# Optimization experiments

Measured on AMD Instinct MI355X. Metric: run time of the kernel, lower is better.

## Reference

```python
import jax, jax.numpy as jnp
import numpy as np

N_QUBITS = 4
N_LAYERS = 3
H_IMG = 512

# ---------- 4-qubit statevector simulator, batched over P patches ----------

def _apply_1q(psi, U, w):
    # shared 2x2 gate U on wire w; psi: (P,2,2,2,2)
    psi = jnp.moveaxis(psi, 1 + w, -1)
    psi = jnp.einsum('ij,...j->...i', U, psi)
    return jnp.moveaxis(psi, -1, 1 + w)

def _apply_1q_batched(psi, U, w):
    # per-patch gate U: (P,2,2)
    psi = jnp.moveaxis(psi, 1 + w, -1)
    psi = jnp.einsum('pij,p...j->p...i', U, psi)
    return jnp.moveaxis(psi, -1, 1 + w)

def _apply_cnot(psi, c, t):
    psi = jnp.moveaxis(psi, (1 + c, 1 + t), (-2, -1))
    top = psi[..., 0:1, :]
    bot = psi[..., 1:2, ::-1]  # X on target when control=1
    psi = jnp.concatenate([top, bot], axis=-2)
    return jnp.moveaxis(psi, (-2, -1), (1 + c, 1 + t))

def _rx(theta):
    # AngleEmbedding default rotation='X'; theta: (P,) -> (P,2,2)
    h = theta * 0.5
    c = jnp.cos(h).astype(jnp.complex64)
    s = (-1j * jnp.sin(h)).astype(jnp.complex64)
    return jnp.stack([jnp.stack([c, s], -1), jnp.stack([s, c], -1)], -2)

def _rot(phi, theta, omega):
    # PennyLane Rot = RZ(omega) RY(theta) RZ(phi)
    c = jnp.cos(theta * 0.5)
    s = jnp.sin(theta * 0.5)
    em = jnp.exp(-0.5j * (phi + omega))
    ep = jnp.exp(0.5j * (phi + omega))
    fm = jnp.exp(0.5j * (phi - omega))
    fp = jnp.exp(-0.5j * (phi - omega))
    row0 = jnp.stack([em * c, -fm * s])
    row1 = jnp.stack([fp * s, ep * c])
    return jnp.stack([row0, row1]).astype(jnp.complex64)

def _qsim(inputs, weights):
    # inputs: (P,4) angles; weights: (3,4,3) Rot params -> (P,4) PauliZ expvals
    P = inputs.shape[0]
    psi = jnp.zeros((P, 2, 2, 2, 2), jnp.complex64).at[:, 0, 0, 0, 0].set(1.0)
    for w in range(N_QUBITS):
        psi = _apply_1q_batched(psi, _rx(inputs[:, w]), w)
    for l in range(N_LAYERS):
        for w in range(N_QUBITS):
            psi = _apply_1q(psi, _rot(weights[l, w, 0], weights[l, w, 1], weights[l, w, 2]), w)
        r = (l % (N_QUBITS - 1)) + 1  # StronglyEntanglingLayers default ranges
        for w in range(N_QUBITS):
            psi = _apply_cnot(psi, w, (w + r) % N_QUBITS)
    probs = psi.real ** 2 + psi.imag ** 2  # (P,2,2,2,2)
    ez = []
    for w in range(N_QUBITS):
        axes = tuple(a for a in range(1, 5) if a != 1 + w)
        p = probs.sum(axes)  # (P,2)
        ez.append(p[:, 0] - p[:, 1])
    return jnp.stack(ez, -1)  # (P,4)

def _qconv(x, q_weights):
    img = x[0, 0]  # (H,W)
    a = img[:-1, :-1]; b = img[:-1, 1:]; c = img[1:, :-1]; d = img[1:, 1:]
    Hm, Wm = a.shape
    patches = jnp.stack([a, b, c, d], -1).reshape(-1, 4)  # row-major 2x2 flatten
    ez = _qsim(patches, q_weights)  # (P,4)
    return ez.reshape(Hm, Wm, 4).transpose(2, 0, 1)[None]  # (1,4,Hm,Wm)

# ---------- classical layers ----------

def _conv(x, w, b):
    y = jax.lax.conv_general_dilated(x, w, (1, 1), 'VALID',
                                     dimension_numbers=('NCHW', 'OIHW', 'NCHW'))
    return y + b[None, :, None, None]

def _maxpool2(x):
    return jax.lax.reduce_window(x, -jnp.inf, jax.lax.max,
                                 (1, 1, 2, 2), (1, 1, 2, 2), 'VALID')

def _adaptive_max(x, out):
    H, W = x.shape[-2], x.shape[-1]
    rows = []
    for i in range(out):
        si, ei = (i * H) // out, -(-((i + 1) * H) // out)
        cols = []
        for j in range(out):
            sj, ej = (j * W) // out, -(-((j + 1) * W) // out)
            cols.append(x[..., si:ei, sj:ej].max((-2, -1)))
        rows.append(jnp.stack(cols, -1))
    return jnp.stack(rows, -2)


def setup_inputs() -> dict:
    key = jax.random.key(0)
    ks = jax.random.split(key, 10)
    x = jax.random.normal(ks[0], (1, 1, H_IMG, H_IMG), jnp.float32)
    q_weights = jax.random.uniform(ks[1], (N_LAYERS, N_QUBITS, 3), jnp.float32,
                                   0.0, 2.0 * np.pi)
    conv2_w = jax.random.normal(ks[2], (20, 4, 5, 5), jnp.float32) * 0.05
    conv2_b = jax.random.normal(ks[3], (20,), jnp.float32) * 0.05
    conv3_w = jax.random.normal(ks[4], (40, 20, 3, 3), jnp.float32) * 0.05
    conv3_b = jax.random.normal(ks[5], (40,), jnp.float32) * 0.05
    fc1_w = jax.random.normal(ks[6], (64, 640), jnp.float32) * 0.05
    fc1_b = jax.random.normal(ks[7], (64,), jnp.float32) * 0.05
    fc2_w = jax.random.normal(ks[8], (10, 64), jnp.float32) * 0.05
    fc2_b = jax.random.normal(ks[9], (10,), jnp.float32) * 0.05
    return {'x': x, 'q_weights': q_weights,
            'conv2_w': conv2_w, 'conv2_b': conv2_b,
            'conv3_w': conv3_w, 'conv3_b': conv3_b,
            'fc1_w': fc1_w, 'fc1_b': fc1_b,
            'fc2_w': fc2_w, 'fc2_b': fc2_b}


def reference(x, q_weights, conv2_w, conv2_b, conv3_w, conv3_b,
              fc1_w, fc1_b, fc2_w, fc2_b):
    h = _maxpool2(jax.nn.sigmoid(_qconv(x, q_weights)))        # (1,4,255,255)
    h = _maxpool2(jax.nn.relu(_conv(h, conv2_w, conv2_b)))      # (1,20,125,125)
    h = _adaptive_max(jax.nn.relu(_conv(h, conv3_w, conv3_b)), 4)  # (1,40,4,4)
    h = h.reshape(-1, 640)
    h = jax.nn.relu(h @ fc1_w.T + fc1_b)
    return h @ fc2_w.T + fc2_b  # (1,10)
```

## Files before the change

### kernel.cpp

```cpp
#include <hip/hip_runtime.h>
#include <math.h>

#define IMG 512
#define QO  255

__global__ void build_M(const float* __restrict__ qw, float2* __restrict__ Mout) {
    __shared__ float2 A[16][16];
    int tid = threadIdx.x;
    for (int e = tid; e < 256; e += 128) {
        int col = e >> 4, row = e & 15;
        A[col][row] = make_float2(col == row ? 1.f : 0.f, 0.f);
    }
    __syncthreads();

    int col = tid >> 3;
    int p   = tid & 7;

    for (int l = 0; l < 3; ++l) {
        for (int w = 0; w < 4; ++w) {
            float phi = qw[(l*4 + w)*3 + 0];
            float th  = qw[(l*4 + w)*3 + 1];
            float om  = qw[(l*4 + w)*3 + 2];
            float ch = cosf(0.5f*th), sh = sinf(0.5f*th);
            float al = 0.5f*(phi + om), be = 0.5f*(phi - om);
            float ca = cosf(al), sa = sinf(al);
            float cb = cosf(be), sb = sinf(be);
            float2 U00 = make_float2( ca*ch, -sa*ch);
            float2 U01 = make_float2(-cb*sh, -sb*sh);
            float2 U10 = make_float2( cb*sh, -sb*sh);
            float2 U11 = make_float2( ca*ch,  sa*ch);

            int bp = 3 - w, m = 1 << bp;
            int low = p & (m - 1);
            int k0  = ((p ^ low) << 1) | low;
            int k1  = k0 | m;
            float2 a0 = A[col][k0], a1 = A[col][k1];
            float2 n0 = make_float2(U00.x*a0.x - U00.y*a0.y + U01.x*a1.x - U01.y*a1.y,
                                    U00.x*a0.y + U00.y*a0.x + U01.x*a1.y + U01.y*a1.x);
            float2 n1 = make_float2(U10.x*a0.x - U10.y*a0.y + U11.x*a1.x - U11.y*a1.y,
                                    U10.x*a0.y + U10.y*a0.x + U11.x*a1.y + U11.y*a1.x);
            A[col][k0] = n0;
            A[col][k1] = n1;
            __syncthreads();
        }
        int r = l % 3 + 1;
        for (int w = 0; w < 4; ++w) {
            int cq = w, tq = (w + r) & 3;
            int bpc = 3 - cq, bpt = 3 - tq;
            if (p < 4) {
                int fr0 = -1, fr1 = -1;
                for (int b = 0; b < 4; ++b) {
                    if (b != bpc && b != bpt) { if (fr0 < 0) fr0 = b; else fr1 = b; }
                }
                int k  = (1 << bpc) | ((p & 1) << fr0) | (((p >> 1) & 1) << fr1);
                int k2 = k | (1 << bpt);
                float2 t = A[col][k]; A[col][k] = A[col][k2]; A[col][k2] = t;
            }
            __syncthreads();
        }
    }

    for (int e = tid; e < 256; e += 128) {
        int row = e >> 4, k = e & 15;
        float2 v = A[k][row];
        int pc = __popc(k) & 3;
        float2 o;
        if      (pc == 0) o = v;
        else if (pc == 1) o = make_float2( v.y, -v.x);
        else if (pc == 2) o = make_float2(-v.x, -v.y);
        else              o = make_float2(-v.y,  v.x);
        Mout[e] = o;
    }
}

__global__ __launch_bounds__(256) void qconv_pool(const float* __restrict__ img,
                                                  const float2* __restrict__ Mg,
                                                  float* __restrict__ out) {
    __shared__ float2 Ms[256];
    int tid = threadIdx.x;
    Ms[tid] = Mg[tid];
    __syncthreads();

    int gid = blockIdx.x * 256 + tid;
    if (gid >= QO * QO) return;
    int i = gid / QO, j = gid - i * QO;
    int r0 = 2 * i, c0col = 2 * j;

    float cs[3][3], sn[3][3];
    #pragma unroll
    for (int rr = 0; rr < 3; ++rr) {
        #pragma unroll
        for (int cc = 0; cc < 3; ++cc) {
            float v = img[(r0 + rr) * IMG + c0col + cc];
            __sincosf(0.5f * v, &sn[rr][cc], &cs[rr][cc]);
        }
    }

    float mx0 = -1e30f, mx1 = -1e30f, mx2 = -1e30f, mx3 = -1e30f;

    #pragma unroll
    for (int pr = 0; pr < 2; ++pr) {
        #pragma unroll
        for (int pc = 0; pc < 2; ++pc) {
            float c0 = cs[pr][pc],     s0 = sn[pr][pc];
            float c1 = cs[pr][pc+1],   s1 = sn[pr][pc+1];
            float c2 = cs[pr+1][pc],   s2 = sn[pr+1][pc];
            float c3 = cs[pr+1][pc+1], s3 = sn[pr+1][pc+1];
            float t01[4] = {c0*c1, c0*s1, s0*c1, s0*s1};
            float t23[4] = {c2*c3, c2*s3, s2*c3, s2*s3};
            float a[16];
            #pragma unroll
            for (int k = 0; k < 16; ++k) a[k] = t01[k >> 2] * t23[k & 3];

            float e0 = 0.f, e1 = 0.f, e2 = 0.f, e3 = 0.f;
            for (int rw = 0; rw < 16; ++rw) {
                float re = 0.f, im = 0.f;
                #pragma unroll
                for (int k = 0; k < 16; ++k) {
                    float2 m = Ms[rw * 16 + k];
                    re = fmaf(m.x, a[k], re);
                    im = fmaf(m.y, a[k], im);
                }
                float pp = re * re + im * im;
                e0 += (rw & 8) ? -pp : pp;
                e1 += (rw & 4) ? -pp : pp;
                e2 += (rw & 2) ? -pp : pp;
                e3 += (rw & 1) ? -pp : pp;
            }
            mx0 = fmaxf(mx0, e0);
            mx1 = fmaxf(mx1, e1);
            mx2 = fmaxf(mx2, e2);
            mx3 = fmaxf(mx3, e3);
        }
    }

    out[0 * QO * QO + gid] = 1.f / (1.f + __expf(-mx0));
    out[1 * QO * QO + gid] = 1.f / (1.f + __expf(-mx1));
    out[2 * QO * QO + gid] = 1.f / (1.f + __expf(-mx2));
    out[3 * QO * QO + gid] = 1.f / (1.f + __expf(-mx3));
}

__global__ __launch_bounds__(256) void conv2_pool(const float* __restrict__ in,
                                                  const float* __restrict__ w,
                                                  const float* __restrict__ b,
                                                  float* __restrict__ out) {
    __shared__ float W[2000];
    __shared__ float B[20];
    for (int e = threadIdx.x; e < 2000; e += 256) W[e] = w[e];
    if (threadIdx.x < 20) B[threadIdx.x] = b[threadIdx.x];
    __syncthreads();

    int gid = blockIdx.x * 256 + threadIdx.x;
    if (gid >= 20 * 125 * 125) return;
    int oc = gid / (125 * 125);
    int rem = gid - oc * 125 * 125;
    int i = rem / 125, j = rem - i * 125;

    float a00 = 0.f, a01 = 0.f, a10 = 0.f, a11 = 0.f;
    for (int ic = 0; ic < 4; ++ic) {
        const float* ip = in + ic * QO * QO + (2 * i) * QO + 2 * j;
        float win[6][6];
        #pragma unroll
        for (int y = 0; y < 6; ++y)
            #pragma unroll
            for (int x = 0; x < 6; ++x)
                win[y][x] = ip[y * QO + x];
        const float* wp = W + (oc * 4 + ic) * 25;
        #pragma unroll
        for (int ky = 0; ky < 5; ++ky) {
            #pragma unroll
            for (int kx = 0; kx < 5; ++kx) {
                float wv = wp[ky * 5 + kx];
                a00 = fmaf(win[ky][kx],     wv, a00);
                a01 = fmaf(win[ky][kx+1],   wv, a01);
                a10 = fmaf(win[ky+1][kx],   wv, a10);
                a11 = fmaf(win[ky+1][kx+1], wv, a11);
            }
        }
    }
    float m = fmaxf(fmaxf(a00, a01), fmaxf(a10, a11));
    out[gid] = fmaxf(m + B[oc], 0.f);
}

__global__ __launch_bounds__(256) void conv3_k(const float* __restrict__ in,
                                               const float* __restrict__ w,
                                               const float* __restrict__ b,
                                               float* __restrict__ out) {
    __shared__ float4 W4[1800];
    for (int e = threadIdx.x; e < 1800; e += 256) {
        int og = e / 180, rr = e - og * 180;
        int base = (og * 4) * 180 + rr;
        W4[e] = make_float4(w[base], w[base + 180], w[base + 360], w[base + 540]);
    }
    __syncthreads();

    int gid = blockIdx.x * 256 + threadIdx.x;
    if (gid >= 10 * 123 * 123) return;
    int og = gid / (123 * 123);
    int rem = gid - og * (123 * 123);
    int y = rem / 123, x = rem - y * 123;
    int oc0 = og * 4;

    float acc0 = 0.f, acc1 = 0.f, acc2 = 0.f, acc3 = 0.f;
    for (int ic = 0; ic < 20; ++ic) {
        const float* ip = in + ic * 125 * 125 + y * 125 + x;
        float v[3][3];
        #pragma unroll
        for (int ky = 0; ky < 3; ++ky)
            #pragma unroll
            for (int kx = 0; kx < 3; ++kx)
                v[ky][kx] = ip[ky * 125 + kx];
        #pragma unroll
        for (int ky = 0; ky < 3; ++ky) {
            #pragma unroll
            for (int kx = 0; kx < 3; ++kx) {
                float4 wv = W4[og * 180 + ic * 9 + ky * 3 + kx];
                float iv = v[ky][kx];
                acc0 = fmaf(iv, wv.x, acc0);
                acc1 = fmaf(iv, wv.y, acc1);
                acc2 = fmaf(iv, wv.z, acc2);
                acc3 = fmaf(iv, wv.w, acc3);
            }
        }
    }
    int sp = y * 123 + x;
    out[(oc0 + 0) * 123 * 123 + sp] = fmaxf(acc0 + b[oc0 + 0], 0.f);
    out[(oc0 + 1) * 123 * 123 + sp] = fmaxf(acc1 + b[oc0 + 1], 0.f);
    out[(oc0 + 2) * 123 * 123 + sp] = fmaxf(acc2 + b[oc0 + 2], 0.f);
    out[(oc0 + 3) * 123 * 123 + sp] = fmaxf(acc3 + b[oc0 + 3], 0.f);
}

__global__ void amax_k(const float* __restrict__ in, float* __restrict__ out) {
    int ob = blockIdx.x;
    int oc = ob >> 4, bi = (ob >> 2) & 3, bj = ob & 3;
    int y0 = (bi * 123) >> 2, y1 = ((bi + 1) * 123 + 3) >> 2;
    int x0 = (bj * 123) >> 2, x1 = ((bj + 1) * 123 + 3) >> 2;
    int ny = y1 - y0, nx = x1 - x0, tot = ny * nx;
    float m = -1e30f;
    for (int e = threadIdx.x; e < tot; e += 64) {
        int yy = e / nx, xx = e - yy * nx;
        m = fmaxf(m, in[oc * 123 * 123 + (y0 + yy) * 123 + x0 + xx]);
    }
    #pragma unroll
    for (int o = 32; o > 0; o >>= 1) m = fmaxf(m, __shfl_down(m, o, 64));
    if (threadIdx.x == 0) out[ob] = m;
}

__global__ void fc_k(const float* __restrict__ h, const float* __restrict__ w1,
                     const float* __restrict__ b1, const float* __restrict__ w2,
                     const float* __restrict__ b2, float* __restrict__ out) {
    __shared__ float hh[640];
    __shared__ float h1[64];
    int t = threadIdx.x;
    for (int e = t; e < 640; e += 64) hh[e] = h[e];
    __syncthreads();
    float acc = b1[t];
    for (int n = 0; n < 640; ++n) acc = fmaf(hh[n], w1[t * 640 + n], acc);
    h1[t] = fmaxf(acc, 0.f);
    __syncthreads();
    if (t < 10) {
        float o = b2[t];
        for (int n = 0; n < 64; ++n) o = fmaf(h1[n], w2[t * 64 + n], o);
        out[t] = o;
    }
}

extern "C" void kernel_launch(void* const* d_in, const int* in_sizes, int n_in,
                              void* d_out, int out_size, void* d_ws, size_t ws_size,
                              hipStream_t stream) {
    const float* x   = (const float*)d_in[0];
    const float* qw  = (const float*)d_in[1];
    const float* c2w = (const float*)d_in[2];
    const float* c2b = (const float*)d_in[3];
    const float* c3w = (const float*)d_in[4];
    const float* c3b = (const float*)d_in[5];
    const float* f1w = (const float*)d_in[6];
    const float* f1b = (const float*)d_in[7];
    const float* f2w = (const float*)d_in[8];
    const float* f2b = (const float*)d_in[9];
    float* out = (float*)d_out;

    float*  wsf   = (float*)d_ws;
    float2* M     = (float2*)d_ws;
    float*  qout  = wsf + 512;
    float*  c2out = qout + 4 * 255 * 255;
    float*  c3out = c2out + 20 * 125 * 125;
    float*  am    = c3out + 40 * 123 * 123;

    build_M<<<1, 128, 0, stream>>>(qw, M);
    qconv_pool<<<(QO * QO + 255) / 256, 256, 0, stream>>>(x, M, qout);
    conv2_pool<<<(20 * 125 * 125 + 255) / 256, 256, 0, stream>>>(qout, c2w, c2b, c2out);
    conv3_k<<<(10 * 123 * 123 + 255) / 256, 256, 0, stream>>>(c2out, c3w, c3b, c3out);
    amax_k<<<640, 64, 0, stream>>>(c3out, am);
    fc_k<<<1, 64, 0, stream>>>(am, f1w, f1b, f2w, f2b, out);
}
```

Baseline: 132.6 us.

## Pad intermediate layouts, read weights uniformly, and register-simulate the circuit matrix

Intermediate feature maps now use padded row strides (256 and 128), so conv2 can issue float2 window loads and rows are aligned. The conv kernels index output channels by blockIdx.y and read weights directly from global memory, where each block's addresses are uniform, replacing the shared-memory staging and its syncs. qconv reads the 16x16 unitary from global instead of LDS. build_M simulates each column in registers with compile-time gates, and fc1 splits each dot product over four lanes with float4 loads. The risk is that global weight reads go through the scalar/L1 path instead of LDS, which may be slower in the hot qconv loop.

```diff
diff --git a/kernel.cpp b/kernel.cpp
--- a/kernel.cpp
+++ b/kernel.cpp
@@ -3,98 +3,92 @@
 
 #define IMG 512
 #define QO  255
+#define QP  256
+#define C2H 125
+#define C2S 128
+#define C3H 123
+#define C3S 128
+
+template<int M_>
+__device__ inline void rot_regs(float2* a, float2 U00, float2 U01, float2 U10, float2 U11) {
+    #pragma unroll
+    for (int s = 0; s < 16; ++s) {
+        if (!(s & M_)) {
+            float2 a0 = a[s], a1 = a[s | M_];
+            a[s]      = make_float2(U00.x*a0.x - U00.y*a0.y + U01.x*a1.x - U01.y*a1.y,
+                                    U00.x*a0.y + U00.y*a0.x + U01.x*a1.y + U01.y*a1.x);
+            a[s | M_] = make_float2(U10.x*a0.x - U10.y*a0.y + U11.x*a1.x - U11.y*a1.y,
+                                    U10.x*a0.y + U10.y*a0.x + U11.x*a1.y + U11.y*a1.x);
+        }
+    }
+}
+template<int MC, int MT>
+__device__ inline void cnot_regs(float2* a) {
+    #pragma unroll
+    for (int s = 0; s < 16; ++s) {
+        if ((s & MC) && !(s & MT)) {
+            float2 t = a[s]; a[s] = a[s | MT]; a[s | MT] = t;
+        }
+    }
+}
+__device__ inline void rot_gate_params(float phi, float th, float om,
+                                       float2& U00, float2& U01, float2& U10, float2& U11) {
+    float ch, sh, ca, sa, cb, sb;
+    __sincosf(0.5f * th, &sh, &ch);
+    __sincosf(0.5f * (phi + om), &sa, &ca);
+    __sincosf(0.5f * (phi - om), &sb, &cb);
+    U00 = make_float2( ca*ch, -sa*ch);
+    U01 = make_float2(-cb*sh, -sb*sh);
+    U10 = make_float2( cb*sh, -sb*sh);
+    U11 = make_float2( ca*ch,  sa*ch);
+}
 
 __global__ void build_M(const float* __restrict__ qw, float2* __restrict__ Mout) {
-    __shared__ float2 A[16][16];
-    int tid = threadIdx.x;
-    for (int e = tid; e < 256; e += 128) {
-        int col = e >> 4, row = e & 15;
-        A[col][row] = make_float2(col == row ? 1.f : 0.f, 0.f);
-    }
-    __syncthreads();
-
-    int col = tid >> 3;
-    int p   = tid & 7;
-
-    for (int l = 0; l < 3; ++l) {
-        for (int w = 0; w < 4; ++w) {
-            float phi = qw[(l*4 + w)*3 + 0];
-            float th  = qw[(l*4 + w)*3 + 1];
-            float om  = qw[(l*4 + w)*3 + 2];
-            float ch = cosf(0.5f*th), sh = sinf(0.5f*th);
-            float al = 0.5f*(phi + om), be = 0.5f*(phi - om);
-            float ca = cosf(al), sa = sinf(al);
-            float cb = cosf(be), sb = sinf(be);
-            float2 U00 = make_float2( ca*ch, -sa*ch);
-            float2 U01 = make_float2(-cb*sh, -sb*sh);
-            float2 U10 = make_float2( cb*sh, -sb*sh);
-            float2 U11 = make_float2( ca*ch,  sa*ch);
-
-            int bp = 3 - w, m = 1 << bp;
-            int low = p & (m - 1);
-            int k0  = ((p ^ low) << 1) | low;
-            int k1  = k0 | m;
-            float2 a0 = A[col][k0], a1 = A[col][k1];
-            float2 n0 = make_float2(U00.x*a0.x - U00.y*a0.y + U01.x*a1.x - U01.y*a1.y,
-                                    U00.x*a0.y + U00.y*a0.x + U01.x*a1.y + U01.y*a1.x);
-            float2 n1 = make_float2(U10.x*a0.x - U10.y*a0.y + U11.x*a1.x - U11.y*a1.y,
-                                    U10.x*a0.y + U10.y*a0.x + U11.x*a1.y + U11.y*a1.x);
-            A[col][k0] = n0;
-            A[col][k1] = n1;
-            __syncthreads();
-        }
-        int r = l % 3 + 1;
-        for (int w = 0; w < 4; ++w) {
-            int cq = w, tq = (w + r) & 3;
-            int bpc = 3 - cq, bpt = 3 - tq;
-            if (p < 4) {
-                int fr0 = -1, fr1 = -1;
-                for (int b = 0; b < 4; ++b) {
-                    if (b != bpc && b != bpt) { if (fr0 < 0) fr0 = b; else fr1 = b; }
-                }
-                int k  = (1 << bpc) | ((p & 1) << fr0) | (((p >> 1) & 1) << fr1);
-                int k2 = k | (1 << bpt);
-                float2 t = A[col][k]; A[col][k] = A[col][k2]; A[col][k2] = t;
-            }
-            __syncthreads();
-        }
-    }
-
-    for (int e = tid; e < 256; e += 128) {
-        int row = e >> 4, k = e & 15;
-        float2 v = A[k][row];
-        int pc = __popc(k) & 3;
-        float2 o;
+    int t = threadIdx.x;
+    if (t >= 16) return;
+    float2 a[16];
+    #pragma unroll
+    for (int s = 0; s < 16; ++s) a[s] = make_float2(s == t ? 1.f : 0.f, 0.f);
+
+    float2 U00, U01, U10, U11;
+#define ROTG(L, W) rot_gate_params(qw[((L)*4+(W))*3+0], qw[((L)*4+(W))*3+1], qw[((L)*4+(W))*3+2], U00,U01,U10,U11); \
+                   rot_regs<(1 << (3-(W)))>(a, U00, U01, U10, U11);
+    ROTG(0,0) ROTG(0,1) ROTG(0,2) ROTG(0,3)
+    cnot_regs<8,4>(a); cnot_regs<4,2>(a); cnot_regs<2,1>(a); cnot_regs<1,8>(a);
+    ROTG(1,0) ROTG(1,1) ROTG(1,2) ROTG(1,3)
+    cnot_regs<8,2>(a); cnot_regs<4,1>(a); cnot_regs<2,8>(a); cnot_regs<1,4>(a);
+    ROTG(2,0) ROTG(2,1) ROTG(2,2) ROTG(2,3)
+    cnot_regs<8,1>(a); cnot_regs<4,8>(a); cnot_regs<2,4>(a); cnot_regs<1,2>(a);
+#undef ROTG
+
+    int pc = __popc(t) & 3;
+    #pragma unroll
+    for (int row = 0; row < 16; ++row) {
+        float2 v = a[row], o;
         if      (pc == 0) o = v;
         else if (pc == 1) o = make_float2( v.y, -v.x);
         else if (pc == 2) o = make_float2(-v.x, -v.y);
         else              o = make_float2(-v.y,  v.x);
-        Mout[e] = o;
+        Mout[row * 16 + t] = o;
     }
 }
 
 __global__ __launch_bounds__(256) void qconv_pool(const float* __restrict__ img,
-                                                  const float2* __restrict__ Mg,
+                                                  const float2* __restrict__ M2,
                                                   float* __restrict__ out) {
-    __shared__ float2 Ms[256];
-    int tid = threadIdx.x;
-    Ms[tid] = Mg[tid];
-    __syncthreads();
-
-    int gid = blockIdx.x * 256 + tid;
+    int gid = blockIdx.x * 256 + threadIdx.x;
     if (gid >= QO * QO) return;
     int i = gid / QO, j = gid - i * QO;
-    int r0 = 2 * i, c0col = 2 * j;
+    int r0 = 2 * i, c0 = 2 * j;
 
     float cs[3][3], sn[3][3];
     #pragma unroll
-    for (int rr = 0; rr < 3; ++rr) {
+    for (int rr = 0; rr < 3; ++rr)
         #pragma unroll
         for (int cc = 0; cc < 3; ++cc) {
-            float v = img[(r0 + rr) * IMG + c0col + cc];
+            float v = img[(r0 + rr) * IMG + c0 + cc];
             __sincosf(0.5f * v, &sn[rr][cc], &cs[rr][cc]);
         }
-    }
 
     float mx0 = -1e30f, mx1 = -1e30f, mx2 = -1e30f, mx3 = -1e30f;
 
@@ -102,26 +96,27 @@
     for (int pr = 0; pr < 2; ++pr) {
         #pragma unroll
         for (int pc = 0; pc < 2; ++pc) {
-            float c0 = cs[pr][pc],     s0 = sn[pr][pc];
-            float c1 = cs[pr][pc+1],   s1 = sn[pr][pc+1];
-            float c2 = cs[pr+1][pc],   s2 = sn[pr+1][pc];
-            float c3 = cs[pr+1][pc+1], s3 = sn[pr+1][pc+1];
-            float t01[4] = {c0*c1, c0*s1, s0*c1, s0*s1};
-            float t23[4] = {c2*c3, c2*s3, s2*c3, s2*s3};
+            float c0v = cs[pr][pc],     s0 = sn[pr][pc];
+            float c1v = cs[pr][pc+1],   s1 = sn[pr][pc+1];
+            float c2v = cs[pr+1][pc],   s2 = sn[pr+1][pc];
+            float c3v = cs[pr+1][pc+1], s3 = sn[pr+1][pc+1];
+            float t01[4] = {c0v*c1v, c0v*s1, s0*c1v, s0*s1};
+            float t23[4] = {c2v*c3v, c2v*s3, s2*c3v, s2*s3};
             float a[16];
             #pragma unroll
             for (int k = 0; k < 16; ++k) a[k] = t01[k >> 2] * t23[k & 3];
 
             float e0 = 0.f, e1 = 0.f, e2 = 0.f, e3 = 0.f;
+            #pragma unroll 4
             for (int rw = 0; rw < 16; ++rw) {
                 float re = 0.f, im = 0.f;
                 #pragma unroll
                 for (int k = 0; k < 16; ++k) {
-                    float2 m = Ms[rw * 16 + k];
+                    float2 m = M2[rw * 16 + k];
                     re = fmaf(m.x, a[k], re);
                     im = fmaf(m.y, a[k], im);
                 }
-                float pp = re * re + im * im;
+                float pp = fmaf(re, re, im * im);
                 e0 += (rw & 8) ? -pp : pp;
                 e1 += (rw & 4) ? -pp : pp;
                 e2 += (rw & 2) ? -pp : pp;
@@ -134,43 +129,42 @@
         }
     }
 
-    out[0 * QO * QO + gid] = 1.f / (1.f + __expf(-mx0));
-    out[1 * QO * QO + gid] = 1.f / (1.f + __expf(-mx1));
-    out[2 * QO * QO + gid] = 1.f / (1.f + __expf(-mx2));
-    out[3 * QO * QO + gid] = 1.f / (1.f + __expf(-mx3));
+    int o = i * QP + j;
+    out[0 * QP * QP + o] = 1.f / (1.f + __expf(-mx0));
+    out[1 * QP * QP + o] = 1.f / (1.f + __expf(-mx1));
+    out[2 * QP * QP + o] = 1.f / (1.f + __expf(-mx2));
+    out[3 * QP * QP + o] = 1.f / (1.f + __expf(-mx3));
 }
 
 __global__ __launch_bounds__(256) void conv2_pool(const float* __restrict__ in,
                                                   const float* __restrict__ w,
                                                   const float* __restrict__ b,
                                                   float* __restrict__ out) {
-    __shared__ float W[2000];
-    __shared__ float B[20];
-    for (int e = threadIdx.x; e < 2000; e += 256) W[e] = w[e];
-    if (threadIdx.x < 20) B[threadIdx.x] = b[threadIdx.x];
-    __syncthreads();
-
-    int gid = blockIdx.x * 256 + threadIdx.x;
-    if (gid >= 20 * 125 * 125) return;
-    int oc = gid / (125 * 125);
-    int rem = gid - oc * 125 * 125;
-    int i = rem / 125, j = rem - i * 125;
+    int oc = blockIdx.y;
+    int sp = blockIdx.x * 256 + threadIdx.x;
+    if (sp >= C2H * C2H) return;
+    int i = sp / C2H, j = sp - i * C2H;
+    const float* wb = w + oc * 100;
 
     float a00 = 0.f, a01 = 0.f, a10 = 0.f, a11 = 0.f;
+    #pragma unroll
     for (int ic = 0; ic < 4; ++ic) {
-        const float* ip = in + ic * QO * QO + (2 * i) * QO + 2 * j;
+        const float* ip = in + ic * QP * QP + (2 * i) * QP + 2 * j;
         float win[6][6];
         #pragma unroll
-        for (int y = 0; y < 6; ++y)
-            #pragma unroll
-            for (int x = 0; x < 6; ++x)
-                win[y][x] = ip[y * QO + x];
-        const float* wp = W + (oc * 4 + ic) * 25;
+        for (int y = 0; y < 6; ++y) {
+            #pragma unroll
+            for (int h = 0; h < 3; ++h) {
+                float2 v = *(const float2*)(ip + y * QP + 2 * h);
+                win[y][2*h]   = v.x;
+                win[y][2*h+1] = v.y;
+            }
+        }
         #pragma unroll
         for (int ky = 0; ky < 5; ++ky) {
             #pragma unroll
             for (int kx = 0; kx < 5; ++kx) {
-                float wv = wp[ky * 5 + kx];
+                float wv = wb[ic * 25 + ky * 5 + kx];
                 a00 = fmaf(win[ky][kx],     wv, a00);
                 a01 = fmaf(win[ky][kx+1],   wv, a01);
                 a10 = fmaf(win[ky+1][kx],   wv, a10);
@@ -179,67 +173,56 @@
         }
     }
     float m = fmaxf(fmaxf(a00, a01), fmaxf(a10, a11));
-    out[gid] = fmaxf(m + B[oc], 0.f);
+    out[oc * C2H * C2S + i * C2S + j] = fmaxf(m + b[oc], 0.f);
 }
 
 __global__ __launch_bounds__(256) void conv3_k(const float* __restrict__ in,
                                                const float* __restrict__ w,
                                                const float* __restrict__ b,
                                                float* __restrict__ out) {
-    __shared__ float4 W4[1800];
-    for (int e = threadIdx.x; e < 1800; e += 256) {
-        int og = e / 180, rr = e - og * 180;
-        int base = (og * 4) * 180 + rr;
-        W4[e] = make_float4(w[base], w[base + 180], w[base + 360], w[base + 540]);
-    }
-    __syncthreads();
-
-    int gid = blockIdx.x * 256 + threadIdx.x;
-    if (gid >= 10 * 123 * 123) return;
-    int og = gid / (123 * 123);
-    int rem = gid - og * (123 * 123);
-    int y = rem / 123, x = rem - y * 123;
+    int og = blockIdx.y;
+    int sp = blockIdx.x * 256 + threadIdx.x;
+    if (sp >= C3H * C3H) return;
+    int y = sp / C3H, x = sp - y * C3H;
     int oc0 = og * 4;
+    const float* wb = w + oc0 * 180;
 
     float acc0 = 0.f, acc1 = 0.f, acc2 = 0.f, acc3 = 0.f;
+    #pragma unroll
     for (int ic = 0; ic < 20; ++ic) {
-        const float* ip = in + ic * 125 * 125 + y * 125 + x;
+        const float* ip = in + ic * C2H * C2S + y * C2S + x;
         float v[3][3];
         #pragma unroll
         for (int ky = 0; ky < 3; ++ky)
             #pragma unroll
             for (int kx = 0; kx < 3; ++kx)
-                v[ky][kx] = ip[ky * 125 + kx];
-        #pragma unroll
-        for (int ky = 0; ky < 3; ++ky) {
-            #pragma unroll
-            for (int kx = 0; kx < 3; ++kx) {
-                float4 wv = W4[og * 180 + ic * 9 + ky * 3 + kx];
-                float iv = v[ky][kx];
-                acc0 = fmaf(iv, wv.x, acc0);
-                acc1 = fmaf(iv, wv.y, acc1);
-                acc2 = fmaf(iv, wv.z, acc2);
-                acc3 = fmaf(iv, wv.w, acc3);
-            }
-        }
-    }
-    int sp = y * 123 + x;
-    out[(oc0 + 0) * 123 * 123 + sp] = fmaxf(acc0 + b[oc0 + 0], 0.f);
-    out[(oc0 + 1) * 123 * 123 + sp] = fmaxf(acc1 + b[oc0 + 1], 0.f);
-    out[(oc0 + 2) * 123 * 123 + sp] = fmaxf(acc2 + b[oc0 + 2], 0.f);
-    out[(oc0 + 3) * 123 * 123 + sp] = fmaxf(acc3 + b[oc0 + 3], 0.f);
+                v[ky][kx] = ip[ky * C2S + kx];
+        #pragma unroll
+        for (int kk = 0; kk < 9; ++kk) {
+            float iv = v[kk / 3][kk % 3];
+            acc0 = fmaf(iv, wb[          ic * 9 + kk], acc0);
+            acc1 = fmaf(iv, wb[180     + ic * 9 + kk], acc1);
+            acc2 = fmaf(iv, wb[360     + ic * 9 + kk], acc2);
+            acc3 = fmaf(iv, wb[540     + ic * 9 + kk], acc3);
+        }
+    }
+    int o = y * C3S + x;
+    out[(oc0 + 0) * C3H * C3S + o] = fmaxf(acc0 + b[oc0 + 0], 0.f);
+    out[(oc0 + 1) * C3H * C3S + o] = fmaxf(acc1 + b[oc0 + 1], 0.f);
+    out[(oc0 + 2) * C3H * C3S + o] = fmaxf(acc2 + b[oc0 + 2], 0.f);
+    out[(oc0 + 3) * C3H * C3S + o] = fmaxf(acc3 + b[oc0 + 3], 0.f);
 }
 
 __global__ void amax_k(const float* __restrict__ in, float* __restrict__ out) {
     int ob = blockIdx.x;
     int oc = ob >> 4, bi = (ob >> 2) & 3, bj = ob & 3;
-    int y0 = (bi * 123) >> 2, y1 = ((bi + 1) * 123 + 3) >> 2;
-    int x0 = (bj * 123) >> 2, x1 = ((bj + 1) * 123 + 3) >> 2;
+    int y0 = (bi * C3H) >> 2, y1 = ((bi + 1) * C3H + 3) >> 2;
+    int x0 = (bj * C3H) >> 2, x1 = ((bj + 1) * C3H + 3) >> 2;
     int ny = y1 - y0, nx = x1 - x0, tot = ny * nx;
     float m = -1e30f;
     for (int e = threadIdx.x; e < tot; e += 64) {
         int yy = e / nx, xx = e - yy * nx;
-        m = fmaxf(m, in[oc * 123 * 123 + (y0 + yy) * 123 + x0 + xx]);
+        m = fmaxf(m, in[oc * C3H * C3S + (y0 + yy) * C3S + x0 + xx]);
     }
     #pragma unroll
     for (int o = 32; o > 0; o >>= 1) m = fmaxf(m, __shfl_down(m, o, 64));
@@ -252,14 +235,29 @@
     __shared__ float hh[640];
     __shared__ float h1[64];
     int t = threadIdx.x;
-    for (int e = t; e < 640; e += 64) hh[e] = h[e];
+    for (int e = t; e < 640; e += 256) hh[e] = h[e];
     __syncthreads();
-    float acc = b1[t];
-    for (int n = 0; n < 640; ++n) acc = fmaf(hh[n], w1[t * 640 + n], acc);
-    h1[t] = fmaxf(acc, 0.f);
+
+    int r = t >> 2, q = t & 3;
+    const float4* wr = (const float4*)(w1 + r * 640 + q * 160);
+    const float*  hp = hh + q * 160;
+    float acc = 0.f;
+    #pragma unroll 4
+    for (int n = 0; n < 40; ++n) {
+        float4 wv = wr[n];
+        acc = fmaf(wv.x, hp[n*4+0], acc);
+        acc = fmaf(wv.y, hp[n*4+1], acc);
+        acc = fmaf(wv.z, hp[n*4+2], acc);
+        acc = fmaf(wv.w, hp[n*4+3], acc);
+    }
+    acc += __shfl_xor(acc, 1, 64);
+    acc += __shfl_xor(acc, 2, 64);
+    if (q == 0) h1[r] = fmaxf(acc + b1[r], 0.f);
     __syncthreads();
+
     if (t < 10) {
         float o = b2[t];
+        #pragma unroll 8
         for (int n = 0; n < 64; ++n) o = fmaf(h1[n], w2[t * 64 + n], o);
         out[t] = o;
     }
@@ -283,14 +281,14 @@
     float*  wsf   = (float*)d_ws;
     float2* M     = (float2*)d_ws;
     float*  qout  = wsf + 512;
-    float*  c2out = qout + 4 * 255 * 255;
-    float*  c3out = c2out + 20 * 125 * 125;
-    float*  am    = c3out + 40 * 123 * 123;
-
-    build_M<<<1, 128, 0, stream>>>(qw, M);
+    float*  c2out = qout + 4 * QP * QP;
+    float*  c3out = c2out + 20 * C2H * C2S;
+    float*  am    = c3out + 40 * C3H * C3S;
+
+    build_M<<<1, 64, 0, stream>>>(qw, M);
     qconv_pool<<<(QO * QO + 255) / 256, 256, 0, stream>>>(x, M, qout);
-    conv2_pool<<<(20 * 125 * 125 + 255) / 256, 256, 0, stream>>>(qout, c2w, c2b, c2out);
-    conv3_k<<<(10 * 123 * 123 + 255) / 256, 256, 0, stream>>>(c2out, c3w, c3b, c3out);
+    conv2_pool<<<dim3((C2H * C2H + 255) / 256, 20), 256, 0, stream>>>(qout, c2w, c2b, c2out);
+    conv3_k<<<dim3((C3H * C3H + 255) / 256, 10), 256, 0, stream>>>(c2out, c3w, c3b, c3out);
     amax_k<<<640, 64, 0, stream>>>(c3out, am);
-    fc_k<<<1, 64, 0, stream>>>(am, f1w, f1b, f2w, f2b, out);
-}
+    fc_k<<<1, 256, 0, stream>>>(am, f1w, f1b, f2w, f2b, out);
+}
```

After: 137.7 us. +3.8%, slower.
